# Optimization experiments

Hardware: AMD Instinct MI355X
Metric: run time of the kernel (lower is better)

## Reference

```python
import jax, jax.numpy as jnp
import numpy as np

IN_DIM = 300   # GloVe embedding dim
MEM = 150      # TreeLSTM memory dim
K = 4          # children per internal node (complete K-ary tree)
D = 9          # number of levels (leaves = level 0, root = level D-1)
SIZES = [K ** (D - 1 - d) for d in range(D)]  # nodes per level, leaves first
N = sum(SIZES)  # 87381 total nodes


def setup_inputs() -> dict:
    key = jax.random.key(0)
    ks = jax.random.split(key, 18)
    s_in = 1.0 / np.sqrt(IN_DIM)
    s_m = 1.0 / np.sqrt(MEM)
    inp = {"embs": jax.random.normal(ks[0], (N, IN_DIM), jnp.float32)}
    i = 1
    for nm in ["ix", "fx", "ux", "ox"]:  # input->mem linears
        inp["W_" + nm] = jax.random.uniform(ks[i], (IN_DIM, MEM), jnp.float32, -s_in, s_in); i += 1
        inp["b_" + nm] = jax.random.uniform(ks[i], (MEM,), jnp.float32, -s_in, s_in); i += 1
    for nm in ["ih", "fh", "uh", "oh"]:  # mem->mem linears
        inp["W_" + nm] = jax.random.uniform(ks[i], (MEM, MEM), jnp.float32, -s_m, s_m); i += 1
        inp["b_" + nm] = jax.random.uniform(ks[i], (MEM,), jnp.float32, -s_m, s_m); i += 1
    return inp


def reference(embs, W_ix, b_ix, W_fx, b_fx, W_ux, b_ux, W_ox, b_ox,
              W_ih, b_ih, W_fh, b_fh, W_uh, b_uh, W_oh, b_oh):
    """Level-batched Child-Sum TreeLSTM over a complete K-ary forest.
    Nodes are stored leaves-first; children of parent p at level d are
    nodes p*K .. p*K+K-1 of level d-1. Returns h for all N nodes (root last)."""
    off = 0
    h_prev = c_prev = None
    h_all = []
    for d in range(D):
        n = SIZES[d]
        x = embs[off:off + n]                       # (n, IN_DIM)
        if d == 0:
            # leaves: zero child state -> child_h_sum = 0, f*child_c = 0
            h_sum = jnp.zeros((n, MEM), embs.dtype)
            fc = jnp.zeros((n, MEM), embs.dtype)
        else:
            ch = h_prev.reshape(n, K, MEM)          # child h, (n, K, MEM)
            cc = c_prev.reshape(n, K, MEM)          # child c
            h_sum = ch.sum(axis=1)                  # child-sum of h
            # per-child forget gate: fh(child_h) + fx(x)
            f = jax.nn.sigmoid(jnp.einsum('nkm,mp->nkp', ch, W_fh) + b_fh
                               + (x @ W_fx + b_fx)[:, None, :])
            fc = (f * cc).sum(axis=1)
        i_g = jax.nn.sigmoid(x @ W_ix + b_ix + h_sum @ W_ih + b_ih)
        o_g = jax.nn.sigmoid(x @ W_ox + b_ox + h_sum @ W_oh + b_oh)
        u = jnp.tanh(x @ W_ux + b_ux + h_sum @ W_uh + b_uh)
        c = i_g * u + fc
        h = o_g * jnp.tanh(c)
        h_all.append(h)
        h_prev, c_prev = h, c
        off += n
    return jnp.concatenate(h_all, axis=0)           # (N, MEM)
```

## Files before the change

### kernel.cpp

```cpp
#include <hip/hip_runtime.h>

#define MEM    150
#define GW     640
#define KX     300
#define KXP    320
#define KH     160
#define NLEAF  65536
#define NTOT   87381
#define DEPTH  9

static const int SIZES[DEPTH] = {65536,16384,4096,1024,256,64,16,4,1};
static const int OFF[DEPTH]   = {0,65536,81920,86016,87040,87296,87360,87376,87380};

typedef __attribute__((ext_vector_type(8))) short short8;
typedef __attribute__((ext_vector_type(4))) float f32x4;

__device__ __forceinline__ float sigf(float x) { return 1.0f / (1.0f + __expf(-x)); }
__device__ __forceinline__ float tanhf_fast(float x) {
    float e = __expf(2.0f * x);
    return 1.0f - 2.0f / (e + 1.0f);
}
__device__ __forceinline__ unsigned short f2bf(float f) {
    union { float f; unsigned u; } v; v.f = f;
    unsigned r = v.u + 0x7FFF + ((v.u >> 16) & 1);
    return (unsigned short)(r >> 16);
}
__device__ __forceinline__ float bf2f(unsigned short u) {
    union { unsigned u; float f; } v; v.u = ((unsigned)u) << 16; return v.f;
}

typedef const __attribute__((address_space(1))) unsigned int* as1_u32p;
typedef __attribute__((address_space(3))) unsigned int* as3_u32p;
__device__ __forceinline__ void gl_lds16(const unsigned short* g, unsigned short* l) {
    __builtin_amdgcn_global_load_lds((as1_u32p)g, (as3_u32p)l, 16, 0, 0);
}

__global__ void prep(const float* __restrict__ Wix, const float* __restrict__ Wfx,
                     const float* __restrict__ Wux, const float* __restrict__ Wox,
                     const float* __restrict__ bix, const float* __restrict__ bfx,
                     const float* __restrict__ bux, const float* __restrict__ box,
                     const float* __restrict__ Wih, const float* __restrict__ Wfh,
                     const float* __restrict__ Wuh, const float* __restrict__ Woh,
                     const float* __restrict__ bfh,
                     const float* __restrict__ embs,
                     unsigned short* __restrict__ W4xT, unsigned short* __restrict__ W4hT,
                     float* __restrict__ b4x, float* __restrict__ b4hf,
                     unsigned short* __restrict__ Abf)
{
    if (blockIdx.x < 256) {
        int tid = blockIdx.x * 256 + threadIdx.x;
        const int stride = 256 * 256;
        for (int idx = tid; idx < GW * KXP; idx += stride) {
            int c = idx / KXP, k = idx - c * KXP;
            int j = c >> 2, g = c & 3;
            const float* W = (g == 0) ? Wix : (g == 1) ? Wfx : (g == 2) ? Wux : Wox;
            W4xT[idx] = (j < MEM && k < KX) ? f2bf(W[k * MEM + j]) : (unsigned short)0;
        }
        for (int idx = tid; idx < GW * KH; idx += stride) {
            int c = idx / KH, k = idx - c * KH;
            int j = c >> 2, g = c & 3;
            const float* W = (g == 0) ? Wih : (g == 1) ? Wfh : (g == 2) ? Wuh : Woh;
            W4hT[idx] = (j < MEM && k < MEM) ? f2bf(W[k * MEM + j]) : (unsigned short)0;
        }
        for (int idx = tid; idx < GW; idx += stride) {
            int j = idx >> 2, g = idx & 3;
            const float* b = (g == 0) ? bix : (g == 1) ? bfx : (g == 2) ? bux : box;
            b4x[idx]  = (j < MEM) ? b[j] : 0.0f;
            b4hf[idx] = (g == 1 && j < MEM) ? bfh[j] : 0.0f;
        }
    } else {
        int idx = (blockIdx.x - 256) * 256 + threadIdx.x;
        if (idx >= NTOT * (KXP / 8)) return;
        int n = idx / (KXP / 8), c = idx - n * (KXP / 8);
        int c0 = c * 8;
        unsigned short v[8];
        if (c0 + 8 <= KX) {
            const float4* p = (const float4*)(embs + (size_t)n * KX + c0);
            float4 f0 = p[0], f1 = p[1];
            v[0]=f2bf(f0.x); v[1]=f2bf(f0.y); v[2]=f2bf(f0.z); v[3]=f2bf(f0.w);
            v[4]=f2bf(f1.x); v[5]=f2bf(f1.y); v[6]=f2bf(f1.z); v[7]=f2bf(f1.w);
        } else {
            const float* row = embs + (size_t)n * KX;
            #pragma unroll
            for (int j = 0; j < 8; ++j) {
                int col = c0 + j;
                v[j] = (col < KX) ? f2bf(row[col]) : (unsigned short)0;
            }
        }
        *(short8*)&Abf[(size_t)n * KXP + c0] = *(short8*)v;
    }
}

__global__ __launch_bounds__(512) void gemm_xproj(
    const unsigned short* __restrict__ A,
    const unsigned short* __restrict__ BT,
    const float* __restrict__ bias,
    unsigned short* __restrict__ PG,
    const float* __restrict__ bih, const float* __restrict__ buh,
    const float* __restrict__ boh,
    float* __restrict__ outLeaf, float* __restrict__ CLeaf,
    unsigned short* __restrict__ HbfLeaf)
{
    __shared__ __align__(16) unsigned short lds[16384];
    unsigned short* As = lds;
    unsigned short* Bs = lds + 8192;

    const int nwg = gridDim.x;
    const int orig = blockIdx.x;
    const int qq = nwg >> 3, rr = nwg & 7;
    const int xcd = orig & 7, lin = orig >> 3;
    const int dd = (xcd < rr ? xcd * (qq + 1) : rr * (qq + 1) + (xcd - rr) * qq) + lin;
    const int mtile = dd / 5, ntile = dd - mtile * 5;

    const int t = threadIdx.x;
    const int m0 = mtile * 128, n0 = ntile * 128;
    const int l = t & 63, w = t >> 6;
    const int l15 = l & 15, q = l >> 4;
    const int wm = (w & 1) * 64, wn = (w >> 1) * 32;

    const int srow = t >> 2;
    const int scol = ((t & 3) ^ (srow & 3)) * 8;
    int gr0 = m0 + srow; if (gr0 >= NTOT) gr0 = NTOT - 1;
    const unsigned short* a0 = A + (size_t)gr0 * KXP + scol;
    const unsigned short* b0 = BT + (size_t)(n0 + srow) * KXP + scol;

    f32x4 acc[4][2];
    #pragma unroll
    for (int i = 0; i < 4; ++i)
        #pragma unroll
        for (int j = 0; j < 2; ++j)
            acc[i][j] = (f32x4){0.f, 0.f, 0.f, 0.f};

    gl_lds16(a0, As + t * 8);
    gl_lds16(b0, Bs + t * 8);

    int cur = 0;
    const int kiters = KXP >> 5;
    for (int kt = 0; kt < kiters; ++kt) {
        if (kt + 1 < kiters) {
            const int ko = (kt + 1) << 5;
            const int nb = cur ^ 1;
            gl_lds16(a0 + ko, As + nb * 4096 + t * 8);
            gl_lds16(b0 + ko, Bs + nb * 4096 + t * 8);
            __builtin_amdgcn_sched_barrier(0);
            asm volatile("s_waitcnt vmcnt(2)" ::: "memory");
        } else {
            asm volatile("s_waitcnt vmcnt(0)" ::: "memory");
        }
        __builtin_amdgcn_s_barrier();
        __builtin_amdgcn_sched_barrier(0);

        short8 a[4], b[2];
        const int csw = (q ^ (l15 & 3)) * 8;
        #pragma unroll
        for (int i = 0; i < 4; ++i)
            a[i] = *(const short8*)&As[cur * 4096 + (wm + i * 16 + l15) * 32 + csw];
        #pragma unroll
        for (int j = 0; j < 2; ++j)
            b[j] = *(const short8*)&Bs[cur * 4096 + (wn + j * 16 + l15) * 32 + csw];
        __builtin_amdgcn_s_setprio(1);
        #pragma unroll
        for (int i = 0; i < 4; ++i)
            #pragma unroll
            for (int j = 0; j < 2; ++j)
                acc[i][j] = __builtin_amdgcn_mfma_f32_16x16x32_bf16(a[i], b[j], acc[i][j], 0, 0, 0);
        __builtin_amdgcn_s_setprio(0);
        __builtin_amdgcn_sched_barrier(0);
        __builtin_amdgcn_s_barrier();
        cur ^= 1;
    }

    float bj[2];
    #pragma unroll
    for (int j = 0; j < 2; ++j) bj[j] = bias[n0 + wn + j * 16 + l15];
    #pragma unroll
    for (int i = 0; i < 4; ++i)
        #pragma unroll
        for (int j = 0; j < 2; ++j)
            #pragma unroll
            for (int r = 0; r < 4; ++r)
                lds[(wm + i * 16 + q * 4 + r) * 128 + wn + j * 16 + l15] =
                    f2bf(acc[i][j][r] + bj[j]);
    __syncthreads();

    if (m0 < NLEAF) {
        #pragma unroll
        for (int s = 0; s < 8; ++s) {
            int idx = (s << 9) + t;
            int row = idx >> 5, jl = idx & 31;
            int grow = m0 + row;
            int j = ntile * 32 + jl;
            const unsigned short* g4 = &lds[row * 128 + jl * 4];
            if (j < MEM) {
                float gi = bf2f(g4[0]) + bih[j];
                float gu = bf2f(g4[2]) + buh[j];
                float go = bf2f(g4[3]) + boh[j];
                float iv = sigf(gi), uv = tanhf_fast(gu), ov = sigf(go);
                float c = iv * uv;
                float h = ov * tanhf_fast(c);
                outLeaf[(size_t)grow * MEM + j] = h;
                CLeaf[(size_t)grow * MEM + j] = c;
                HbfLeaf[(size_t)grow * KH + j] = f2bf(h);
            } else if (j < KH) {
                HbfLeaf[(size_t)grow * KH + j] = 0;
            }
        }
    } else {
        int row = t >> 2, qd = t & 3;
        int grow = m0 + row;
        if (grow < NTOT) {
            const unsigned short* src = &lds[row * 128 + qd * 32];
            unsigned short* dst = PG + (size_t)grow * GW + n0 + qd * 32;
            #pragma unroll
            for (int c8 = 0; c8 < 4; ++c8)
                *(short8*)(dst + c8 * 8) = *(const short8*)(src + c8 * 8);
        }
    }
}

__global__ __launch_bounds__(512) void gemm_level(
    const unsigned short* __restrict__ Hprev, int nprev, int npar,
    const unsigned short* __restrict__ BT, const float* __restrict__ bias,
    const unsigned short* __restrict__ P,
    const float* __restrict__ Cprev,
    const float* __restrict__ bih, const float* __restrict__ buh,
    const float* __restrict__ boh,
    float* __restrict__ outRow, float* __restrict__ Crow,
    unsigned short* __restrict__ HbfRow)
{
    __shared__ __align__(16) unsigned short lds[16384];
    unsigned short* As = lds;
    unsigned short* Bs = lds + 8192;

    const int nwg = gridDim.x;
    const int orig = blockIdx.x;
    const int qq = nwg >> 3, rr = nwg & 7;
    const int xcd = orig & 7, lin = orig >> 3;
    const int dd = (xcd < rr ? xcd * (qq + 1) : rr * (qq + 1) + (xcd - rr) * qq) + lin;
    const int mtile = dd / 5, ntile = dd - mtile * 5;

    const int t = threadIdx.x;
    const int m0 = mtile * 128, n0 = ntile * 128;
    const int l = t & 63, w = t >> 6;
    const int l15 = l & 15, q = l >> 4;
    const int wm = (w & 1) * 64, wn = (w >> 1) * 32;

    const int srow = t >> 2;
    const int scol = ((t & 3) ^ (srow & 3)) * 8;
    int gr0 = m0 + srow; if (gr0 >= nprev) gr0 = nprev - 1;
    const unsigned short* a0 = Hprev + (size_t)gr0 * KH + scol;
    const unsigned short* b0 = BT + (size_t)(n0 + srow) * KH + scol;

    f32x4 acc[4][2];
    #pragma unroll
    for (int i = 0; i < 4; ++i)
        #pragma unroll
        for (int j = 0; j < 2; ++j)
            acc[i][j] = (f32x4){0.f, 0.f, 0.f, 0.f};

    gl_lds16(a0, As + t * 8);
    gl_lds16(b0, Bs + t * 8);

    int cur = 0;
    const int kiters = KH >> 5;
    for (int kt = 0; kt < kiters; ++kt) {
        if (kt + 1 < kiters) {
            const int ko = (kt + 1) << 5;
            const int nb = cur ^ 1;
            gl_lds16(a0 + ko, As + nb * 4096 + t * 8);
            gl_lds16(b0 + ko, Bs + nb * 4096 + t * 8);
            __builtin_amdgcn_sched_barrier(0);
            asm volatile("s_waitcnt vmcnt(2)" ::: "memory");
        } else {
            asm volatile("s_waitcnt vmcnt(0)" ::: "memory");
        }
        __builtin_amdgcn_s_barrier();
        __builtin_amdgcn_sched_barrier(0);

        short8 a[4], b[2];
        const int csw = (q ^ (l15 & 3)) * 8;
        #pragma unroll
        for (int i = 0; i < 4; ++i)
            a[i] = *(const short8*)&As[cur * 4096 + (wm + i * 16 + l15) * 32 + csw];
        #pragma unroll
        for (int j = 0; j < 2; ++j)
            b[j] = *(const short8*)&Bs[cur * 4096 + (wn + j * 16 + l15) * 32 + csw];
        __builtin_amdgcn_s_setprio(1);
        #pragma unroll
        for (int i = 0; i < 4; ++i)
            #pragma unroll
            for (int j = 0; j < 2; ++j)
                acc[i][j] = __builtin_amdgcn_mfma_f32_16x16x32_bf16(a[i], b[j], acc[i][j], 0, 0, 0);
        __builtin_amdgcn_s_setprio(0);
        __builtin_amdgcn_sched_barrier(0);
        __builtin_amdgcn_s_barrier();
        cur ^= 1;
    }

    float bj[2];
    #pragma unroll
    for (int j = 0; j < 2; ++j) bj[j] = bias[n0 + wn + j * 16 + l15];
    #pragma unroll
    for (int i = 0; i < 4; ++i)
        #pragma unroll
        for (int j = 0; j < 2; ++j)
            #pragma unroll
            for (int r = 0; r < 4; ++r)
                lds[(wm + i * 16 + q * 4 + r) * 128 + wn + j * 16 + l15] =
                    f2bf(acc[i][j][r] + bj[j]);
    __syncthreads();

    const int pp0 = m0 >> 2;
    #pragma unroll
    for (int s = 0; s < 2; ++s) {
        int idx = (s << 9) + t;
        int pl = idx >> 5, jl = idx & 31;
        int par = pp0 + pl;
        if (par >= npar) continue;
        int j = ntile * 32 + jl;
        if (j < MEM) {
            const unsigned short* xr = P + (size_t)par * GW + 4 * j;
            float ip = bf2f(xr[0]) + bih[j];
            float fx = bf2f(xr[1]);
            float up = bf2f(xr[2]) + buh[j];
            float op = bf2f(xr[3]) + boh[j];
            float fc = 0.0f;
            #pragma unroll
            for (int k = 0; k < 4; ++k) {
                const unsigned short* g4 = &lds[(pl * 4 + k) * 128 + jl * 4];
                ip += bf2f(g4[0]);
                up += bf2f(g4[2]);
                op += bf2f(g4[3]);
                float f = sigf(fx + bf2f(g4[1]));
                fc += f * Cprev[(size_t)(4 * par + k) * MEM + j];
            }
            float iv = sigf(ip), uv = tanhf_fast(up), ov = sigf(op);
            float c = iv * uv + fc;
            float h = ov * tanhf_fast(c);
            outRow[(size_t)par * MEM + j] = h;
            Crow[(size_t)par * MEM + j] = c;
            HbfRow[(size_t)par * KH + j] = f2bf(h);
        } else if (j < KH) {
            HbfRow[(size_t)par * KH + j] = 0;
        }
    }
}

extern "C" void kernel_launch(void* const* d_in, const int* in_sizes, int n_in,
                              void* d_out, int out_size, void* d_ws, size_t ws_size,
                              hipStream_t stream)
{
    (void)in_sizes; (void)n_in; (void)out_size;
    const float* embs = (const float*)d_in[0];
    const float* Wix = (const float*)d_in[1];  const float* bix = (const float*)d_in[2];
    const float* Wfx = (const float*)d_in[3];  const float* bfx = (const float*)d_in[4];
    const float* Wux = (const float*)d_in[5];  const float* bux = (const float*)d_in[6];
    const float* Wox = (const float*)d_in[7];  const float* box = (const float*)d_in[8];
    const float* Wih = (const float*)d_in[9];  const float* bih = (const float*)d_in[10];
    const float* Wfh = (const float*)d_in[11]; const float* bfh = (const float*)d_in[12];
    const float* Wuh = (const float*)d_in[13]; const float* buh = (const float*)d_in[14];
    const float* Woh = (const float*)d_in[15]; const float* boh = (const float*)d_in[16];
    float* out = (float*)d_out;

    char* p = (char*)d_ws;
    auto alloc = [&](size_t bytes) -> char* {
        char* r = p;
        p += (bytes + 255) & ~(size_t)255;
        return r;
    };
    unsigned short* PG   = (unsigned short*)alloc((size_t)NTOT * GW * 2);
    float*          C    = (float*)alloc((size_t)NTOT * MEM * 4);
    unsigned short* Hbf  = (unsigned short*)alloc((size_t)NTOT * KH * 2);
    unsigned short* W4xT = (unsigned short*)alloc((size_t)GW * KXP * 2);
    unsigned short* W4hT = (unsigned short*)alloc((size_t)GW * KH * 2);
    float*          b4x  = (float*)alloc(GW * 4);
    float*          b4hf = (float*)alloc(GW * 4);
    if ((size_t)(p - (char*)d_ws) > ws_size) return;

    unsigned short* Abf = PG;

    {
        int convBlocks = (NTOT * (KXP / 8) + 255) / 256;
        prep<<<256 + convBlocks, 256, 0, stream>>>(
            Wix, Wfx, Wux, Wox, bix, bfx, bux, box,
            Wih, Wfh, Wuh, Woh, bfh, embs,
            W4xT, W4hT, b4x, b4hf, Abf);
    }

    {
        int mt = (NTOT + 127) / 128;
        gemm_xproj<<<mt * 5, 512, 0, stream>>>(
            Abf, W4xT, b4x, PG, bih, buh, boh, out, C, Hbf);
    }

    for (int d = 1; d < DEPTH; ++d) {
        int nprev = SIZES[d - 1];
        int n = SIZES[d];
        int mt = (nprev + 127) / 128;
        gemm_level<<<mt * 5, 512, 0, stream>>>(
            Hbf + (size_t)OFF[d - 1] * KH, nprev, n,
            W4hT, b4hf,
            PG + (size_t)OFF[d] * GW,
            C + (size_t)OFF[d - 1] * MEM,
            bih, buh, boh,
            out + (size_t)OFF[d] * MEM, C + (size_t)OFF[d] * MEM,
            Hbf + (size_t)OFF[d] * KH);
    }
}
```

Baseline: 345.5 us.

## Triple-buffer LDS k-tiles and strengthen swizzle in both GEMM kernels

Both the input-projection GEMM and the per-level GEMM move from double-buffered to triple-buffered LDS staging. Two k-tiles are prefetched ahead and the vmcnt waits are adjusted to match, so global loads get more time to land behind the MFMAs. The LDS XOR swizzle now also folds in row bits 2-3 to cut bank conflicts on fragment reads. LDS use per block grows from 32KB to 48KB, which may lower occupancy, and the level GEMM has only 5 k-steps, so it gains little pipelining depth.

```diff
diff --git a/kernel.cpp b/kernel.cpp
--- a/kernel.cpp
+++ b/kernel.cpp
@@ -101,9 +101,9 @@
     float* __restrict__ outLeaf, float* __restrict__ CLeaf,
     unsigned short* __restrict__ HbfLeaf)
 {
-    __shared__ __align__(16) unsigned short lds[16384];
+    __shared__ __align__(16) unsigned short lds[24576];
     unsigned short* As = lds;
-    unsigned short* Bs = lds + 8192;
+    unsigned short* Bs = lds + 12288;
 
     const int nwg = gridDim.x;
     const int orig = blockIdx.x;
@@ -119,7 +119,8 @@
     const int wm = (w & 1) * 64, wn = (w >> 1) * 32;
 
     const int srow = t >> 2;
-    const int scol = ((t & 3) ^ (srow & 3)) * 8;
+    const int sx = (srow ^ (srow >> 2)) & 3;
+    const int scol = ((t & 3) ^ sx) * 8;
     int gr0 = m0 + srow; if (gr0 >= NTOT) gr0 = NTOT - 1;
     const unsigned short* a0 = A + (size_t)gr0 * KXP + scol;
     const unsigned short* b0 = BT + (size_t)(n0 + srow) * KXP + scol;
@@ -131,18 +132,24 @@
         for (int j = 0; j < 2; ++j)
             acc[i][j] = (f32x4){0.f, 0.f, 0.f, 0.f};
 
-    gl_lds16(a0, As + t * 8);
-    gl_lds16(b0, Bs + t * 8);
-
-    int cur = 0;
-    const int kiters = KXP >> 5;
-    for (int kt = 0; kt < kiters; ++kt) {
-        if (kt + 1 < kiters) {
-            const int ko = (kt + 1) << 5;
-            const int nb = cur ^ 1;
-            gl_lds16(a0 + ko, As + nb * 4096 + t * 8);
-            gl_lds16(b0 + ko, Bs + nb * 4096 + t * 8);
+    const int NST = KXP >> 5;
+    gl_lds16(a0,      As + t * 8);
+    gl_lds16(b0,      Bs + t * 8);
+    gl_lds16(a0 + 32, As + 4096 + t * 8);
+    gl_lds16(b0 + 32, Bs + 4096 + t * 8);
+
+    const int csw = ((q ^ (l15 & 3) ^ (l15 >> 2)) & 3) * 8;
+
+    #pragma unroll
+    for (int kt = 0; kt < NST; ++kt) {
+        if (kt + 2 < NST) {
+            const int s = kt + 2;
+            const int bi = s - (s / 3) * 3;
+            gl_lds16(a0 + s * 32, As + bi * 4096 + t * 8);
+            gl_lds16(b0 + s * 32, Bs + bi * 4096 + t * 8);
             __builtin_amdgcn_sched_barrier(0);
+            asm volatile("s_waitcnt vmcnt(4)" ::: "memory");
+        } else if (kt + 1 < NST) {
             asm volatile("s_waitcnt vmcnt(2)" ::: "memory");
         } else {
             asm volatile("s_waitcnt vmcnt(0)" ::: "memory");
@@ -150,14 +157,14 @@
         __builtin_amdgcn_s_barrier();
         __builtin_amdgcn_sched_barrier(0);
 
+        const int cb = kt - (kt / 3) * 3;
         short8 a[4], b[2];
-        const int csw = (q ^ (l15 & 3)) * 8;
         #pragma unroll
         for (int i = 0; i < 4; ++i)
-            a[i] = *(const short8*)&As[cur * 4096 + (wm + i * 16 + l15) * 32 + csw];
-        #pragma unroll
-        for (int j = 0; j < 2; ++j)
-            b[j] = *(const short8*)&Bs[cur * 4096 + (wn + j * 16 + l15) * 32 + csw];
+            a[i] = *(const short8*)&As[cb * 4096 + (wm + i * 16 + l15) * 32 + csw];
+        #pragma unroll
+        for (int j = 0; j < 2; ++j)
+            b[j] = *(const short8*)&Bs[cb * 4096 + (wn + j * 16 + l15) * 32 + csw];
         __builtin_amdgcn_s_setprio(1);
         #pragma unroll
         for (int i = 0; i < 4; ++i)
@@ -167,7 +174,6 @@
         __builtin_amdgcn_s_setprio(0);
         __builtin_amdgcn_sched_barrier(0);
         __builtin_amdgcn_s_barrier();
-        cur ^= 1;
     }
 
     float bj[2];
@@ -228,9 +234,9 @@
     float* __restrict__ outRow, float* __restrict__ Crow,
     unsigned short* __restrict__ HbfRow)
 {
-    __shared__ __align__(16) unsigned short lds[16384];
+    __shared__ __align__(16) unsigned short lds[24576];
     unsigned short* As = lds;
-    unsigned short* Bs = lds + 8192;
+    unsigned short* Bs = lds + 12288;
 
     const int nwg = gridDim.x;
     const int orig = blockIdx.x;
@@ -246,7 +252,8 @@
     const int wm = (w & 1) * 64, wn = (w >> 1) * 32;
 
     const int srow = t >> 2;
-    const int scol = ((t & 3) ^ (srow & 3)) * 8;
+    const int sx = (srow ^ (srow >> 2)) & 3;
+    const int scol = ((t & 3) ^ sx) * 8;
     int gr0 = m0 + srow; if (gr0 >= nprev) gr0 = nprev - 1;
     const unsigned short* a0 = Hprev + (size_t)gr0 * KH + scol;
     const unsigned short* b0 = BT + (size_t)(n0 + srow) * KH + scol;
@@ -258,18 +265,24 @@
         for (int j = 0; j < 2; ++j)
             acc[i][j] = (f32x4){0.f, 0.f, 0.f, 0.f};
 
-    gl_lds16(a0, As + t * 8);
-    gl_lds16(b0, Bs + t * 8);
-
-    int cur = 0;
-    const int kiters = KH >> 5;
-    for (int kt = 0; kt < kiters; ++kt) {
-        if (kt + 1 < kiters) {
-            const int ko = (kt + 1) << 5;
-            const int nb = cur ^ 1;
-            gl_lds16(a0 + ko, As + nb * 4096 + t * 8);
-            gl_lds16(b0 + ko, Bs + nb * 4096 + t * 8);
+    const int NST = KH >> 5;
+    gl_lds16(a0,      As + t * 8);
+    gl_lds16(b0,      Bs + t * 8);
+    gl_lds16(a0 + 32, As + 4096 + t * 8);
+    gl_lds16(b0 + 32, Bs + 4096 + t * 8);
+
+    const int csw = ((q ^ (l15 & 3) ^ (l15 >> 2)) & 3) * 8;
+
+    #pragma unroll
+    for (int kt = 0; kt < NST; ++kt) {
+        if (kt + 2 < NST) {
+            const int s = kt + 2;
+            const int bi = s - (s / 3) * 3;
+            gl_lds16(a0 + s * 32, As + bi * 4096 + t * 8);
+            gl_lds16(b0 + s * 32, Bs + bi * 4096 + t * 8);
             __builtin_amdgcn_sched_barrier(0);
+            asm volatile("s_waitcnt vmcnt(4)" ::: "memory");
+        } else if (kt + 1 < NST) {
             asm volatile("s_waitcnt vmcnt(2)" ::: "memory");
         } else {
             asm volatile("s_waitcnt vmcnt(0)" ::: "memory");
@@ -277,14 +290,14 @@
         __builtin_amdgcn_s_barrier();
         __builtin_amdgcn_sched_barrier(0);
 
+        const int cb = kt - (kt / 3) * 3;
         short8 a[4], b[2];
-        const int csw = (q ^ (l15 & 3)) * 8;
         #pragma unroll
         for (int i = 0; i < 4; ++i)
-            a[i] = *(const short8*)&As[cur * 4096 + (wm + i * 16 + l15) * 32 + csw];
-        #pragma unroll
-        for (int j = 0; j < 2; ++j)
-            b[j] = *(const short8*)&Bs[cur * 4096 + (wn + j * 16 + l15) * 32 + csw];
+            a[i] = *(const short8*)&As[cb * 4096 + (wm + i * 16 + l15) * 32 + csw];
+        #pragma unroll
+        for (int j = 0; j < 2; ++j)
+            b[j] = *(const short8*)&Bs[cb * 4096 + (wn + j * 16 + l15) * 32 + csw];
         __builtin_amdgcn_s_setprio(1);
         #pragma unroll
         for (int i = 0; i < 4; ++i)
@@ -294,7 +307,6 @@
         __builtin_amdgcn_s_setprio(0);
         __builtin_amdgcn_sched_barrier(0);
         __builtin_amdgcn_s_barrier();
-        cur ^= 1;
     }
 
     float bj[2];
```

Measured after the change: 347.4 us. About the same (+0.6%).
